# Optimization experiments

Hardware: AMD Instinct MI355X
Metric: run time of the kernel (lower is better)

Reference implementation:

```python
import jax, jax.numpy as jnp
import numpy as np

N = 100000   # nodes
E = 1600000  # edges (avg degree 16)
D = 64       # din == dout
L = 4        # n_layers
EPS = 1e-5   # pyg LayerNorm eps


def setup_inputs() -> dict:
    key = jax.random.key(0)
    k = jax.random.split(key, 4)
    x = jax.random.normal(k[0], (N, D), dtype=jnp.float32)
    edge_index = jax.random.randint(k[1], (2, E), 0, N, dtype=jnp.int32)
    Ws = jax.random.normal(k[2], (L, D, D), dtype=jnp.float32) * (1.0 / np.sqrt(D))
    bs = jnp.zeros((L, D), dtype=jnp.float32)
    ln_w = jnp.ones((L, D), dtype=jnp.float32)
    ln_b = jnp.zeros((L, D), dtype=jnp.float32)
    return {"x": x, "edge_index": edge_index, "Ws": Ws, "bs": bs, "ln_w": ln_w, "ln_b": ln_b}


def reference(x, edge_index, Ws, bs, ln_w, ln_b):
    src, dst = edge_index[0], edge_index[1]
    n = x.shape[0]
    # GCN symmetric normalization with self-loops: deg = 1 + in-degree
    deg = jnp.zeros((n,), x.dtype).at[dst].add(1.0) + 1.0
    dinv = jax.lax.rsqrt(deg)                       # [N]
    enorm = (dinv[src] * dinv[dst])[:, None]        # [E,1]
    self_norm = (dinv * dinv)[:, None]              # [N,1]

    h = x
    for l in range(Ws.shape[0]):
        hw = h @ Ws[l]                              # [N,D]
        # gather-normalize-scatter neighborhood aggregation + self-loop term
        agg = jnp.zeros_like(hw).at[dst].add(enorm * hw[src])
        agg = agg + self_norm * hw + bs[l]
        # pyg LayerNorm (mode='graph', batch=None): mean/var over all nodes+channels
        mean = jnp.mean(agg)
        var = jnp.mean(jnp.square(agg - mean))
        hn = ln_w[l] * (agg - mean) * jax.lax.rsqrt(var + EPS) + ln_b[l]
        h = jax.nn.relu(hn)                         # dropout p=0.0 -> identity
    return h
```

## Files before the change

### kernel.cpp

```cpp
#include <hip/hip_runtime.h>

#define DD 64
#define NBUCK 256
#define BSTRIDE 32
#define CAP 13312
#define GSTRIDE 16
#define TILE 4096
#define BSLACK 8192

__device__ __forceinline__ unsigned pack_bf16_2(float a, float b) {
  unsigned ua = __float_as_uint(a);
  unsigned ub = __float_as_uint(b);
  unsigned ra = (ua + 0x7FFFu + ((ua >> 16) & 1u)) >> 16;
  unsigned rb = (ub + 0x7FFFu + ((ub >> 16) & 1u)) >> 16;
  return ra | (rb << 16);
}

__device__ __forceinline__ float4 unpack_bf16_4(uint2 p) {
  float4 f;
  f.x = __uint_as_float(p.x << 16);
  f.y = __uint_as_float(p.x & 0xFFFF0000u);
  f.z = __uint_as_float(p.y << 16);
  f.w = __uint_as_float(p.y & 0xFFFF0000u);
  return f;
}

__device__ __forceinline__ void ln_stats(const double* __restrict__ buckets, int M,
                                         float* mean_out, float* rstd_out) {
  __shared__ double ra[4], rb[4];
  __shared__ float sm[2];
  int t = threadIdx.x;
  double a = buckets[(size_t)t * BSTRIDE];
  double b = buckets[(size_t)t * BSTRIDE + 1];
#pragma unroll
  for (int o = 1; o <= 32; o <<= 1) {
    a += __shfl_xor(a, o);
    b += __shfl_xor(b, o);
  }
  if ((t & 63) == 0) { ra[t >> 6] = a; rb[t >> 6] = b; }
  __syncthreads();
  if (t == 0) {
    double s1 = ra[0] + ra[1] + ra[2] + ra[3];
    double s2 = rb[0] + rb[1] + rb[2] + rb[3];
    double mean = s1 / M;
    double var = s2 / M - mean * mean;
    sm[0] = (float)mean;
    sm[1] = (float)rsqrt(var + 1e-5);
  }
  __syncthreads();
  *mean_out = sm[0];
  *rstd_out = sm[1];
}


__global__ __launch_bounds__(256) void init_gcur_k(int* __restrict__ gcur, int nbkt) {
  int t = blockIdx.x * 256 + threadIdx.x;
  if (t < nbkt) gcur[t * GSTRIDE] = t * CAP;
}

__global__ __launch_bounds__(256) void bucket_a_k(const int* __restrict__ src, const int* __restrict__ dst,
                                                  int* __restrict__ gcur, unsigned* __restrict__ slots, int E) {
  __shared__ int hist[256], cur[256], hbase[256];
  int t = threadIdx.x;
  hist[t] = 0;
  cur[t] = 0;
  __syncthreads();
  int t0 = blockIdx.x * TILE;
  unsigned pk[16];
  int bk[16];
#pragma unroll
  for (int k = 0; k < 16; ++k) {
    int e = t0 + k * 256 + t;
    if (e < E) {
      int s = src[e], d = dst[e];
      bk[k] = d >> 9;
      pk[k] = (unsigned)s | ((unsigned)(d & 511) << 17);
      atomicAdd(&hist[bk[k]], 1);
    } else {
      bk[k] = -1;
      pk[k] = 0;
    }
  }
  __syncthreads();
  if (hist[t] > 0) hbase[t] = atomicAdd(&gcur[t * GSTRIDE], hist[t]);
  __syncthreads();
#pragma unroll
  for (int k = 0; k < 16; ++k) {
    if (bk[k] >= 0) {
      int r = atomicAdd(&cur[bk[k]], 1);
      slots[(size_t)hbase[bk[k]] + r] = pk[k];
    }
  }
}

__global__ __launch_bounds__(256) void scan_nb_k(const int* __restrict__ gcur, int* __restrict__ bbase, int nbkt) {
  __shared__ int ts[256];
  int t = threadIdx.x;
  int c = (t < nbkt) ? (gcur[t * GSTRIDE] - t * CAP) : 0;
  ts[t] = c;
  __syncthreads();
  for (int o = 1; o < 256; o <<= 1) {
    int u = (t >= o) ? ts[t - o] : 0;
    __syncthreads();
    ts[t] += u;
    __syncthreads();
  }
  if (t < nbkt) bbase[t] = ts[t] - c;
}

__global__ __launch_bounds__(256) void bucket_b_k(const unsigned* __restrict__ slots,
                                                  const int* __restrict__ gcur, const int* __restrict__ bbase,
                                                  int2* __restrict__ off2, float* __restrict__ dinv,
                                                  int* __restrict__ csr, int N) {
  __shared__ int hist[512], excl[512], ts[256];
  int b = blockIdx.x, t = threadIdx.x;
  int base = b * CAP;
  int cnt = gcur[b * GSTRIDE] - base;
  if (cnt > CAP) cnt = CAP;
  int cbase = bbase[b] + b * BSLACK;
  int node0 = b << 9;
  hist[t] = 0;
  hist[t + 256] = 0;
  __syncthreads();
  for (int i = t; i < cnt; i += 256) atomicAdd(&hist[slots[(size_t)base + i] >> 17], 1);
  __syncthreads();
  int h0 = hist[2 * t], h1 = hist[2 * t + 1];
  int p0 = (h0 + 15) & ~15, p1 = (h1 + 15) & ~15;
  int pair = p0 + p1;
  ts[t] = pair;
  __syncthreads();
  for (int o = 1; o < 256; o <<= 1) {
    int u = (t >= o) ? ts[t - o] : 0;
    __syncthreads();
    ts[t] += u;
    __syncthreads();
  }
  int ep = ts[t] - pair;
  int start0 = cbase + ep, start1 = cbase + ep + p0;
  int j0 = node0 + 2 * t, j1 = j0 + 1;
  if (j0 < N) { off2[j0] = make_int2(start0, start0 + p0); dinv[j0] = rsqrtf((float)h0 + 1.0f); }
  if (j1 < N) { off2[j1] = make_int2(start1, start1 + p1); dinv[j1] = rsqrtf((float)h1 + 1.0f); }
  excl[2 * t] = start0;
  excl[2 * t + 1] = start1;
  __syncthreads();
  for (int i = t; i < cnt; i += 256) {
    unsigned e = slots[(size_t)base + i];
    int pos = atomicAdd(&excl[e >> 17], 1);
    csr[pos] = (int)(e & 0x1FFFFu);
  }
  __syncthreads();
  for (int i = h0; i < p0; ++i) csr[start0 + i] = N;
  for (int i = h1; i < p1; ++i) csr[start1 + i] = N;
}


__global__ __launch_bounds__(256) void gemm_ln_k(const float* __restrict__ in, const float* __restrict__ W,
                                                 uint4* __restrict__ hwb, const float* __restrict__ dinv,
                                                 const float* __restrict__ lnw, const float* __restrict__ lnb,
                                                 const double* __restrict__ buckets, int M,
                                                 int applyLn, int n) {
  __shared__ float Wl[64 * 64];
  __shared__ float Al[64 * 68];
  int t = threadIdx.x;
  float mean = 0.f, rstd = 1.f;
  if (applyLn) ln_stats(buckets, M, &mean, &rstd);
#pragma unroll
  for (int i = 0; i < 4; ++i)
    ((float4*)Wl)[t + i * 256] = ((const float4*)W)[t + i * 256];
  int row0 = blockIdx.x * 64;
#pragma unroll
  for (int i = 0; i < 4; ++i) {
    int q = t + i * 256;
    int r = q >> 4, c4 = q & 15;
    int gr = row0 + r;
    float4 v = make_float4(0.f, 0.f, 0.f, 0.f);
    if (gr < n) v = ((const float4*)in)[(size_t)gr * 16 + c4];
    if (applyLn) {
      int c = c4 * 4;
      v.x = fmaxf(fmaf((v.x - mean) * rstd, lnw[c + 0], lnb[c + 0]), 0.f);
      v.y = fmaxf(fmaf((v.y - mean) * rstd, lnw[c + 1], lnb[c + 1]), 0.f);
      v.z = fmaxf(fmaf((v.z - mean) * rstd, lnw[c + 2], lnb[c + 2]), 0.f);
      v.w = fmaxf(fmaf((v.w - mean) * rstd, lnw[c + 3], lnb[c + 3]), 0.f);
    }
    *(float4*)&Al[r * 68 + c4 * 4] = v;
  }
  __syncthreads();
  int r = t >> 2, cb = (t & 3) * 16;
  float acc[16];
#pragma unroll
  for (int j = 0; j < 16; ++j) acc[j] = 0.f;
  for (int k = 0; k < 64; ++k) {
    float a = Al[r * 68 + k];
#pragma unroll
    for (int j = 0; j < 16; ++j) acc[j] = fmaf(a, Wl[k * 64 + cb + j], acc[j]);
  }
  int gr = row0 + r;
  if (gr < n) {
    float di = dinv[gr];
#pragma unroll
    for (int j = 0; j < 16; ++j) acc[j] *= di;
    uint4 u0, u1;
    u0.x = pack_bf16_2(acc[0], acc[1]);
    u0.y = pack_bf16_2(acc[2], acc[3]);
    u0.z = pack_bf16_2(acc[4], acc[5]);
    u0.w = pack_bf16_2(acc[6], acc[7]);
    u1.x = pack_bf16_2(acc[8], acc[9]);
    u1.y = pack_bf16_2(acc[10], acc[11]);
    u1.z = pack_bf16_2(acc[12], acc[13]);
    u1.w = pack_bf16_2(acc[14], acc[15]);
    hwb[(size_t)gr * 8 + (t & 3) * 2 + 0] = u0;
    hwb[(size_t)gr * 8 + (t & 3) * 2 + 1] = u1;
  }
}

__global__ __launch_bounds__(256) void agg_k(const uint2* __restrict__ hwb, const int2* __restrict__ off2,
                                             const int* __restrict__ csr, const float* __restrict__ dinv,
                                             const float4* __restrict__ bias4, float4* __restrict__ out4,
                                             double* __restrict__ buckets, int n) {
  int t = threadIdx.x;
  int lane = t & 63;
  int w = t >> 6;
  int g = lane >> 4, q = lane & 15;
  int wbase = (blockIdx.x * 4 + w) * 8;
  float s1 = 0.f, s2 = 0.f;
#pragma unroll 1
  for (int ni = 0; ni < 8; ++ni) {
    int wid = wbase + ni;
    if (wid >= n) break;
    int2 oo = off2[wid];
    float4 acc = make_float4(0.f, 0.f, 0.f, 0.f);
    if (g == 0) acc = unpack_bf16_4(hwb[(size_t)wid * 16 + q]);
    for (int base = oo.x; base < oo.y; base += 16) {
      int4 c = *(const int4*)(csr + base + g * 4);
      float4 v0 = unpack_bf16_4(hwb[(size_t)c.x * 16 + q]);
      float4 v1 = unpack_bf16_4(hwb[(size_t)c.y * 16 + q]);
      float4 v2 = unpack_bf16_4(hwb[(size_t)c.z * 16 + q]);
      float4 v3 = unpack_bf16_4(hwb[(size_t)c.w * 16 + q]);
      float ax = v0.x + v1.x, bx = v2.x + v3.x;
      float ay = v0.y + v1.y, by = v2.y + v3.y;
      float az = v0.z + v1.z, bz = v2.z + v3.z;
      float aw = v0.w + v1.w, bw = v2.w + v3.w;
      acc.x += ax + bx;
      acc.y += ay + by;
      acc.z += az + bz;
      acc.w += aw + bw;
    }
#pragma unroll
    for (int o = 16; o <= 32; o <<= 1) {
      acc.x += __shfl_xor(acc.x, o);
      acc.y += __shfl_xor(acc.y, o);
      acc.z += __shfl_xor(acc.z, o);
      acc.w += __shfl_xor(acc.w, o);
    }
    if (g == 0) {
      float dd = dinv[wid];
      float4 b = bias4[q];
      acc.x = fmaf(dd, acc.x, b.x);
      acc.y = fmaf(dd, acc.y, b.y);
      acc.z = fmaf(dd, acc.z, b.z);
      acc.w = fmaf(dd, acc.w, b.w);
      out4[(size_t)wid * 16 + q] = acc;
      s1 += acc.x + acc.y + acc.z + acc.w;
      s2 += acc.x * acc.x + acc.y * acc.y + acc.z * acc.z + acc.w * acc.w;
    }
  }
#pragma unroll
  for (int o = 1; o <= 32; o <<= 1) {
    s1 += __shfl_xor(s1, o);
    s2 += __shfl_xor(s2, o);
  }
  __shared__ float red1[4], red2[4];
  if (lane == 0) { red1[w] = s1; red2[w] = s2; }
  __syncthreads();
  if (t == 0) {
    double a = (double)red1[0] + (double)red1[1] + (double)red1[2] + (double)red1[3];
    double b = (double)red2[0] + (double)red2[1] + (double)red2[2] + (double)red2[3];
    double* bp = buckets + (size_t)(blockIdx.x & (NBUCK - 1)) * BSTRIDE;
    atomicAdd(&bp[0], a);
    atomicAdd(&bp[1], b);
  }
}

__global__ __launch_bounds__(256) void norm_relu_k(float4* __restrict__ io, const float* __restrict__ lnw,
                                                   const float* __restrict__ lnb,
                                                   const double* __restrict__ buckets, int M, int n4) {
  float mean, rstd;
  ln_stats(buckets, M, &mean, &rstd);
  for (int i = blockIdx.x * 256 + threadIdx.x; i < n4; i += gridDim.x * 256) {
    float4 v = io[i];
    int c = (i & 15) * 4;
    v.x = fmaxf(fmaf((v.x - mean) * rstd, lnw[c + 0], lnb[c + 0]), 0.f);
    v.y = fmaxf(fmaf((v.y - mean) * rstd, lnw[c + 1], lnb[c + 1]), 0.f);
    v.z = fmaxf(fmaf((v.z - mean) * rstd, lnw[c + 2], lnb[c + 2]), 0.f);
    v.w = fmaxf(fmaf((v.w - mean) * rstd, lnw[c + 3], lnb[c + 3]), 0.f);
    io[i] = v;
  }
}


extern "C" void kernel_launch(void* const* d_in, const int* in_sizes, int n_in,
                              void* d_out, int out_size, void* d_ws, size_t ws_size,
                              hipStream_t stream) {
  const float* x = (const float*)d_in[0];
  const int* ei = (const int*)d_in[1];
  const float* Ws = (const float*)d_in[2];
  const float* bs = (const float*)d_in[3];
  const float* lnw = (const float*)d_in[4];
  const float* lnb = (const float*)d_in[5];
  float* out = (float*)d_out;

  const int N = in_sizes[0] / DD;
  const int E = in_sizes[1] / 2;
  const int L = in_sizes[2] / (DD * DD);
  const int* srcp = ei;
  const int* dstp = ei + E;
  const int nbkt = (N + 511) >> 9;

  char* p = (char*)d_ws;
  size_t ofs = 0;
  auto carve = [&](size_t bytes) -> void* {
    void* r = p + ofs;
    ofs = (ofs + bytes + 255) & ~(size_t)255;
    return r;
  };
  int* gcur = (int*)carve((size_t)256 * GSTRIDE * 4);
  int* bbase = (int*)carve((size_t)256 * 4);
  unsigned* slots = (unsigned*)carve((size_t)256 * CAP * 4);
  double* buckets = (double*)carve((size_t)NBUCK * BSTRIDE * 8 * 4);
  int2* off2 = (int2*)carve((size_t)N * 8);
  float* dinv = (float*)carve((size_t)N * 4);
  int* csr = (int*)carve(((size_t)E + (size_t)nbkt * BSLACK + 64) * 4);
  uint4* hwb = (uint4*)carve((size_t)(N + 1) * DD * 2);

  hipMemsetAsync(buckets, 0, (size_t)NBUCK * BSTRIDE * 8 * 4, stream);
  hipMemsetAsync(hwb + (size_t)N * 8, 0, DD * 2, stream);

  init_gcur_k<<<1, 256, 0, stream>>>(gcur, nbkt);
  int nTiles = (E + TILE - 1) / TILE;
  bucket_a_k<<<nTiles, 256, 0, stream>>>(srcp, dstp, gcur, slots, E);
  scan_nb_k<<<1, 256, 0, stream>>>(gcur, bbase, nbkt);
  bucket_b_k<<<nbkt, 256, 0, stream>>>(slots, gcur, bbase, off2, dinv, csr, N);

  int gGemm = (N + 63) / 64;
  int gAgg = (N + 31) / 32;
  for (int l = 0; l < L; ++l) {
    const float* in = (l == 0) ? x : out;
    const float* plnw = (l == 0) ? lnw : lnw + (l - 1) * DD;
    const float* plnb = (l == 0) ? lnb : lnb + (l - 1) * DD;
    const double* pbuck = buckets + (size_t)((l == 0) ? 0 : (l - 1)) * NBUCK * BSTRIDE;
    gemm_ln_k<<<gGemm, 256, 0, stream>>>(in, Ws + (size_t)l * DD * DD, hwb, dinv, plnw, plnb,
                                         pbuck, N * DD, (l > 0) ? 1 : 0, N);
    double* lbuck = buckets + (size_t)l * NBUCK * BSTRIDE;
    agg_k<<<gAgg, 256, 0, stream>>>((const uint2*)hwb, off2, csr, dinv,
                                    (const float4*)(bs + (size_t)l * DD), (float4*)out,
                                    lbuck, N);
  }
  norm_relu_k<<<1024, 256, 0, stream>>>((float4*)out, lnw + (size_t)(L - 1) * DD,
                                        lnb + (size_t)(L - 1) * DD,
                                        buckets + (size_t)(L - 1) * NBUCK * BSTRIDE,
                                        N * DD, N * (DD / 4));
}
```

Measured before the change: 360.5 us.

## Fold self-loop into CSR and aggregate two nodes per wave concurrently

The CSR build now writes each node's own index into its padded neighbor list, so the self-loop term is gathered like any other neighbor instead of being loaded separately. The aggregation kernel handles two destination nodes per iteration with interleaved gather loops, doubling the independent memory loads in flight to hide gather latency. Bias is loaded once per thread. The change adds padding per node, and masked lanes still issue dummy gathers of the padding row when one node finishes before the other.

After: 386.9 us. 7.3% more time.

```diff
diff --git a/kernel.cpp b/kernel.cpp
--- a/kernel.cpp
+++ b/kernel.cpp
@@ -125,7 +125,7 @@
   for (int i = t; i < cnt; i += 256) atomicAdd(&hist[slots[(size_t)base + i] >> 17], 1);
   __syncthreads();
   int h0 = hist[2 * t], h1 = hist[2 * t + 1];
-  int p0 = (h0 + 15) & ~15, p1 = (h1 + 15) & ~15;
+  int p0 = (h0 + 16) & ~15, p1 = (h1 + 16) & ~15;
   int pair = p0 + p1;
   ts[t] = pair;
   __syncthreads();
@@ -149,8 +149,10 @@
     csr[pos] = (int)(e & 0x1FFFFu);
   }
   __syncthreads();
-  for (int i = h0; i < p0; ++i) csr[start0 + i] = N;
-  for (int i = h1; i < p1; ++i) csr[start1 + i] = N;
+  csr[start0 + h0] = (j0 < N) ? j0 : N;
+  for (int i = h0 + 1; i < p0; ++i) csr[start0 + i] = N;
+  csr[start1 + h1] = (j1 < N) ? j1 : N;
+  for (int i = h1 + 1; i < p1; ++i) csr[start1 + i] = N;
 }
 
 
@@ -223,45 +225,75 @@
   int g = lane >> 4, q = lane & 15;
   int wbase = (blockIdx.x * 4 + w) * 8;
   float s1 = 0.f, s2 = 0.f;
+  float4 bq = bias4[q];
 #pragma unroll 1
-  for (int ni = 0; ni < 8; ++ni) {
-    int wid = wbase + ni;
-    if (wid >= n) break;
-    int2 oo = off2[wid];
-    float4 acc = make_float4(0.f, 0.f, 0.f, 0.f);
-    if (g == 0) acc = unpack_bf16_4(hwb[(size_t)wid * 16 + q]);
-    for (int base = oo.x; base < oo.y; base += 16) {
-      int4 c = *(const int4*)(csr + base + g * 4);
-      float4 v0 = unpack_bf16_4(hwb[(size_t)c.x * 16 + q]);
-      float4 v1 = unpack_bf16_4(hwb[(size_t)c.y * 16 + q]);
-      float4 v2 = unpack_bf16_4(hwb[(size_t)c.z * 16 + q]);
-      float4 v3 = unpack_bf16_4(hwb[(size_t)c.w * 16 + q]);
-      float ax = v0.x + v1.x, bx = v2.x + v3.x;
-      float ay = v0.y + v1.y, by = v2.y + v3.y;
-      float az = v0.z + v1.z, bz = v2.z + v3.z;
-      float aw = v0.w + v1.w, bw = v2.w + v3.w;
-      acc.x += ax + bx;
-      acc.y += ay + by;
-      acc.z += az + bz;
-      acc.w += aw + bw;
+  for (int pr = 0; pr < 4; ++pr) {
+    int wid0 = wbase + 2 * pr;
+    int wid1 = wid0 + 1;
+    if (wid0 >= n) break;
+    int4 oo;
+    if (wid1 < n) {
+      oo = *(const int4*)(off2 + wid0);
+    } else {
+      int2 o0 = off2[wid0];
+      oo = make_int4(o0.x, o0.y, 0, 0);
+    }
+    float4 a0 = make_float4(0.f, 0.f, 0.f, 0.f);
+    float4 a1 = make_float4(0.f, 0.f, 0.f, 0.f);
+    int b0 = oo.x, e0 = oo.y, b1 = oo.z, e1 = oo.w;
+    while (b0 < e0 || b1 < e1) {
+      bool d0 = b0 < e0, d1 = b1 < e1;
+      int4 c0 = d0 ? *(const int4*)(csr + b0 + g * 4) : make_int4(n, n, n, n);
+      int4 c1 = d1 ? *(const int4*)(csr + b1 + g * 4) : make_int4(n, n, n, n);
+      float4 u00 = unpack_bf16_4(hwb[(size_t)c0.x * 16 + q]);
+      float4 u01 = unpack_bf16_4(hwb[(size_t)c0.y * 16 + q]);
+      float4 u02 = unpack_bf16_4(hwb[(size_t)c0.z * 16 + q]);
+      float4 u03 = unpack_bf16_4(hwb[(size_t)c0.w * 16 + q]);
+      float4 u10 = unpack_bf16_4(hwb[(size_t)c1.x * 16 + q]);
+      float4 u11 = unpack_bf16_4(hwb[(size_t)c1.y * 16 + q]);
+      float4 u12 = unpack_bf16_4(hwb[(size_t)c1.z * 16 + q]);
+      float4 u13 = unpack_bf16_4(hwb[(size_t)c1.w * 16 + q]);
+      a0.x += (u00.x + u01.x) + (u02.x + u03.x);
+      a0.y += (u00.y + u01.y) + (u02.y + u03.y);
+      a0.z += (u00.z + u01.z) + (u02.z + u03.z);
+      a0.w += (u00.w + u01.w) + (u02.w + u03.w);
+      a1.x += (u10.x + u11.x) + (u12.x + u13.x);
+      a1.y += (u10.y + u11.y) + (u12.y + u13.y);
+      a1.z += (u10.z + u11.z) + (u12.z + u13.z);
+      a1.w += (u10.w + u11.w) + (u12.w + u13.w);
+      if (d0) b0 += 16;
+      if (d1) b1 += 16;
     }
 #pragma unroll
     for (int o = 16; o <= 32; o <<= 1) {
-      acc.x += __shfl_xor(acc.x, o);
-      acc.y += __shfl_xor(acc.y, o);
-      acc.z += __shfl_xor(acc.z, o);
-      acc.w += __shfl_xor(acc.w, o);
+      a0.x += __shfl_xor(a0.x, o);
+      a0.y += __shfl_xor(a0.y, o);
+      a0.z += __shfl_xor(a0.z, o);
+      a0.w += __shfl_xor(a0.w, o);
+      a1.x += __shfl_xor(a1.x, o);
+      a1.y += __shfl_xor(a1.y, o);
+      a1.z += __shfl_xor(a1.z, o);
+      a1.w += __shfl_xor(a1.w, o);
     }
     if (g == 0) {
-      float dd = dinv[wid];
-      float4 b = bias4[q];
-      acc.x = fmaf(dd, acc.x, b.x);
-      acc.y = fmaf(dd, acc.y, b.y);
-      acc.z = fmaf(dd, acc.z, b.z);
-      acc.w = fmaf(dd, acc.w, b.w);
-      out4[(size_t)wid * 16 + q] = acc;
-      s1 += acc.x + acc.y + acc.z + acc.w;
-      s2 += acc.x * acc.x + acc.y * acc.y + acc.z * acc.z + acc.w * acc.w;
+      float dd0 = dinv[wid0];
+      a0.x = fmaf(dd0, a0.x, bq.x);
+      a0.y = fmaf(dd0, a0.y, bq.y);
+      a0.z = fmaf(dd0, a0.z, bq.z);
+      a0.w = fmaf(dd0, a0.w, bq.w);
+      out4[(size_t)wid0 * 16 + q] = a0;
+      s1 += a0.x + a0.y + a0.z + a0.w;
+      s2 += a0.x * a0.x + a0.y * a0.y + a0.z * a0.z + a0.w * a0.w;
+      if (wid1 < n) {
+        float dd1 = dinv[wid1];
+        a1.x = fmaf(dd1, a1.x, bq.x);
+        a1.y = fmaf(dd1, a1.y, bq.y);
+        a1.z = fmaf(dd1, a1.z, bq.z);
+        a1.w = fmaf(dd1, a1.w, bq.w);
+        out4[(size_t)wid1 * 16 + q] = a1;
+        s1 += a1.x + a1.y + a1.z + a1.w;
+        s2 += a1.x * a1.x + a1.y * a1.y + a1.z * a1.z + a1.w * a1.w;
+      }
     }
   }
 #pragma unroll
```

## Use bf16 MFMA for the per-layer GEMM and memset the bucket cursors

Applied to the files above, without the earlier changes.

Replaces the FP32 shared-memory FMA GEMM with a bf16 MFMA 16x16x32 kernel. Each wave converts its input rows (after LayerNorm and ReLU) and the weight matrix into bf16 register fragments, then stages the output through LDS so it can be written to global memory with coalesced stores. Separately, the init_gcur kernel launch is replaced by a hipMemsetAsync, with bucket cursors now counting from zero and the base offset added where they are used. Rounding the GEMM inputs to bf16 loses precision, and every wave reloads W with strided global loads.

Result: faster. 311.8 us (-13.5%).

```diff
diff --git a/kernel.cpp b/kernel.cpp
--- a/kernel.cpp
+++ b/kernel.cpp
@@ -8,12 +8,20 @@
 #define TILE 4096
 #define BSLACK 8192
 
+typedef __attribute__((ext_vector_type(8))) short bf16x8;
+typedef __attribute__((ext_vector_type(4))) float f32x4;
+
 __device__ __forceinline__ unsigned pack_bf16_2(float a, float b) {
   unsigned ua = __float_as_uint(a);
   unsigned ub = __float_as_uint(b);
   unsigned ra = (ua + 0x7FFFu + ((ua >> 16) & 1u)) >> 16;
   unsigned rb = (ub + 0x7FFFu + ((ub >> 16) & 1u)) >> 16;
   return ra | (rb << 16);
+}
+
+__device__ __forceinline__ unsigned short f2bf(float f) {
+  unsigned u = __float_as_uint(f);
+  return (unsigned short)((u + 0x7FFFu + ((u >> 16) & 1u)) >> 16);
 }
 
 __device__ __forceinline__ float4 unpack_bf16_4(uint2 p) {
@@ -52,11 +60,6 @@
   *rstd_out = sm[1];
 }
 
-
-__global__ __launch_bounds__(256) void init_gcur_k(int* __restrict__ gcur, int nbkt) {
-  int t = blockIdx.x * 256 + threadIdx.x;
-  if (t < nbkt) gcur[t * GSTRIDE] = t * CAP;
-}
 
 __global__ __launch_bounds__(256) void bucket_a_k(const int* __restrict__ src, const int* __restrict__ dst,
                                                   int* __restrict__ gcur, unsigned* __restrict__ slots, int E) {
@@ -82,7 +85,7 @@
     }
   }
   __syncthreads();
-  if (hist[t] > 0) hbase[t] = atomicAdd(&gcur[t * GSTRIDE], hist[t]);
+  if (hist[t] > 0) hbase[t] = t * CAP + atomicAdd(&gcur[t * GSTRIDE], hist[t]);
   __syncthreads();
 #pragma unroll
   for (int k = 0; k < 16; ++k) {
@@ -96,7 +99,7 @@
 __global__ __launch_bounds__(256) void scan_nb_k(const int* __restrict__ gcur, int* __restrict__ bbase, int nbkt) {
   __shared__ int ts[256];
   int t = threadIdx.x;
-  int c = (t < nbkt) ? (gcur[t * GSTRIDE] - t * CAP) : 0;
+  int c = (t < nbkt) ? gcur[t * GSTRIDE] : 0;
   ts[t] = c;
   __syncthreads();
   for (int o = 1; o < 256; o <<= 1) {
@@ -115,7 +118,7 @@
   __shared__ int hist[512], excl[512], ts[256];
   int b = blockIdx.x, t = threadIdx.x;
   int base = b * CAP;
-  int cnt = gcur[b * GSTRIDE] - base;
+  int cnt = gcur[b * GSTRIDE];
   if (cnt > CAP) cnt = CAP;
   int cbase = bbase[b] + b * BSLACK;
   int node0 = b << 9;
@@ -154,62 +157,79 @@
 }
 
 
-__global__ __launch_bounds__(256) void gemm_ln_k(const float* __restrict__ in, const float* __restrict__ W,
-                                                 uint4* __restrict__ hwb, const float* __restrict__ dinv,
-                                                 const float* __restrict__ lnw, const float* __restrict__ lnb,
-                                                 const double* __restrict__ buckets, int M,
-                                                 int applyLn, int n) {
-  __shared__ float Wl[64 * 64];
-  __shared__ float Al[64 * 68];
-  int t = threadIdx.x;
+__global__ __launch_bounds__(256) void gemm_mfma_k(const float* __restrict__ in, const float* __restrict__ W,
+                                                   uint4* __restrict__ hwb, const float* __restrict__ dinv,
+                                                   const float* __restrict__ lnw, const float* __restrict__ lnb,
+                                                   const double* __restrict__ buckets, int M,
+                                                   int applyLn, int n) {
+  __shared__ unsigned short ctile[4][16][72];
+  int t = threadIdx.x;
+  int w = t >> 6, lane = t & 63;
+  int lm = lane & 15, lk = lane >> 4;
   float mean = 0.f, rstd = 1.f;
   if (applyLn) ln_stats(buckets, M, &mean, &rstd);
-#pragma unroll
-  for (int i = 0; i < 4; ++i)
-    ((float4*)Wl)[t + i * 256] = ((const float4*)W)[t + i * 256];
-  int row0 = blockIdx.x * 64;
-#pragma unroll
-  for (int i = 0; i < 4; ++i) {
-    int q = t + i * 256;
-    int r = q >> 4, c4 = q & 15;
-    int gr = row0 + r;
-    float4 v = make_float4(0.f, 0.f, 0.f, 0.f);
-    if (gr < n) v = ((const float4*)in)[(size_t)gr * 16 + c4];
+
+  bf16x8 bfrag[2][4];
+#pragma unroll
+  for (int ks = 0; ks < 2; ++ks)
+#pragma unroll
+    for (int ct = 0; ct < 4; ++ct) {
+      bf16x8 bb;
+      int col = ct * 16 + lm;
+      int kb = ks * 32 + lk * 8;
+#pragma unroll
+      for (int j = 0; j < 8; ++j) bb[j] = (short)f2bf(W[(kb + j) * 64 + col]);
+      bfrag[ks][ct] = bb;
+    }
+
+  int row = blockIdx.x * 64 + w * 16 + lm;
+  bool valid = row < n;
+  bf16x8 afrag[2];
+#pragma unroll
+  for (int ks = 0; ks < 2; ++ks) {
+    float4 v0 = make_float4(0.f, 0.f, 0.f, 0.f), v1 = v0;
+    if (valid) {
+      const float4* ip = (const float4*)in + (size_t)row * 16 + ks * 8 + lk * 2;
+      v0 = ip[0];
+      v1 = ip[1];
+    }
+    float vals[8] = {v0.x, v0.y, v0.z, v0.w, v1.x, v1.y, v1.z, v1.w};
     if (applyLn) {
-      int c = c4 * 4;
-      v.x = fmaxf(fmaf((v.x - mean) * rstd, lnw[c + 0], lnb[c + 0]), 0.f);
-      v.y = fmaxf(fmaf((v.y - mean) * rstd, lnw[c + 1], lnb[c + 1]), 0.f);
-      v.z = fmaxf(fmaf((v.z - mean) * rstd, lnw[c + 2], lnb[c + 2]), 0.f);
-      v.w = fmaxf(fmaf((v.w - mean) * rstd, lnw[c + 3], lnb[c + 3]), 0.f);
-    }
-    *(float4*)&Al[r * 68 + c4 * 4] = v;
-  }
-  __syncthreads();
-  int r = t >> 2, cb = (t & 3) * 16;
-  float acc[16];
-#pragma unroll
-  for (int j = 0; j < 16; ++j) acc[j] = 0.f;
-  for (int k = 0; k < 64; ++k) {
-    float a = Al[r * 68 + k];
-#pragma unroll
-    for (int j = 0; j < 16; ++j) acc[j] = fmaf(a, Wl[k * 64 + cb + j], acc[j]);
-  }
-  int gr = row0 + r;
-  if (gr < n) {
-    float di = dinv[gr];
-#pragma unroll
-    for (int j = 0; j < 16; ++j) acc[j] *= di;
-    uint4 u0, u1;
-    u0.x = pack_bf16_2(acc[0], acc[1]);
-    u0.y = pack_bf16_2(acc[2], acc[3]);
-    u0.z = pack_bf16_2(acc[4], acc[5]);
-    u0.w = pack_bf16_2(acc[6], acc[7]);
-    u1.x = pack_bf16_2(acc[8], acc[9]);
-    u1.y = pack_bf16_2(acc[10], acc[11]);
-    u1.z = pack_bf16_2(acc[12], acc[13]);
-    u1.w = pack_bf16_2(acc[14], acc[15]);
-    hwb[(size_t)gr * 8 + (t & 3) * 2 + 0] = u0;
-    hwb[(size_t)gr * 8 + (t & 3) * 2 + 1] = u1;
+      int cb = ks * 32 + lk * 8;
+#pragma unroll
+      for (int j = 0; j < 8; ++j)
+        vals[j] = fmaxf(fmaf((vals[j] - mean) * rstd, lnw[cb + j], lnb[cb + j]), 0.f);
+    }
+    bf16x8 aa;
+#pragma unroll
+    for (int j = 0; j < 8; ++j) aa[j] = (short)f2bf(vals[j]);
+    afrag[ks] = aa;
+  }
+
+  f32x4 acc[4];
+#pragma unroll
+  for (int ct = 0; ct < 4; ++ct) acc[ct] = (f32x4){0.f, 0.f, 0.f, 0.f};
+#pragma unroll
+  for (int ks = 0; ks < 2; ++ks)
+#pragma unroll
+    for (int ct = 0; ct < 4; ++ct)
+      acc[ct] = __builtin_amdgcn_mfma_f32_16x16x32_bf16(afrag[ks], bfrag[ks][ct], acc[ct], 0, 0, 0);
+
+#pragma unroll
+  for (int r = 0; r < 4; ++r) {
+    int grow = blockIdx.x * 64 + w * 16 + lk * 4 + r;
+    float di = (grow < n) ? dinv[grow] : 0.f;
+#pragma unroll
+    for (int ct = 0; ct < 4; ++ct)
+      ctile[w][lk * 4 + r][ct * 16 + lm] = f2bf(acc[ct][r] * di);
+  }
+  __syncthreads();
+  int srow = lane >> 2, sq = lane & 3;
+  int grow = blockIdx.x * 64 + w * 16 + srow;
+  if (grow < n) {
+    const uint4* lp = (const uint4*)&ctile[w][srow][sq * 16];
+    hwb[(size_t)grow * 8 + sq * 2 + 0] = lp[0];
+    hwb[(size_t)grow * 8 + sq * 2 + 1] = lp[1];
   }
 }
 
@@ -332,10 +352,10 @@
   int* csr = (int*)carve(((size_t)E + (size_t)nbkt * BSLACK + 64) * 4);
   uint4* hwb = (uint4*)carve((size_t)(N + 1) * DD * 2);
 
+  hipMemsetAsync(gcur, 0, (size_t)256 * GSTRIDE * 4, stream);
   hipMemsetAsync(buckets, 0, (size_t)NBUCK * BSTRIDE * 8 * 4, stream);
   hipMemsetAsync(hwb + (size_t)N * 8, 0, DD * 2, stream);
 
-  init_gcur_k<<<1, 256, 0, stream>>>(gcur, nbkt);
   int nTiles = (E + TILE - 1) / TILE;
   bucket_a_k<<<nTiles, 256, 0, stream>>>(srcp, dstp, gcur, slots, E);
   scan_nb_k<<<1, 256, 0, stream>>>(gcur, bbase, nbkt);
@@ -348,8 +368,8 @@
     const float* plnw = (l == 0) ? lnw : lnw + (l - 1) * DD;
     const float* plnb = (l == 0) ? lnb : lnb + (l - 1) * DD;
     const double* pbuck = buckets + (size_t)((l == 0) ? 0 : (l - 1)) * NBUCK * BSTRIDE;
-    gemm_ln_k<<<gGemm, 256, 0, stream>>>(in, Ws + (size_t)l * DD * DD, hwb, dinv, plnw, plnb,
-                                         pbuck, N * DD, (l > 0) ? 1 : 0, N);
+    gemm_mfma_k<<<gGemm, 256, 0, stream>>>(in, Ws + (size_t)l * DD * DD, hwb, dinv, plnw, plnb,
+                                           pbuck, N * DD, (l > 0) ? 1 : 0, N);
     double* lbuck = buckets + (size_t)l * NBUCK * BSTRIDE;
     agg_k<<<gAgg, 256, 0, stream>>>((const uint2*)hwb, off2, csr, dinv,
                                     (const float4*)(bs + (size_t)l * DD), (float4*)out,
```
